# Performance work log

Hardware: AMD Instinct MI355X
Metric: run time of the kernel (lower is better)

The kernel has to match this reference:

```python
import jax, jax.numpy as jnp
import numpy as np

N = 20000
E = 320000
IN_DIM = 128
HID = 64
HEADS = 8
OUT_DIM = 128
NEG_SLOPE = 0.2  # PyG GATConv default leaky_relu slope


def _glorot(key, shape):
    fan_in = shape[0] if len(shape) > 1 else shape[-1]
    return jax.random.normal(key, shape, dtype=jnp.float32) / jnp.sqrt(jnp.float32(fan_in))


def setup_inputs() -> dict:
    key = jax.random.key(0)
    ks = jax.random.split(key, 16)
    x = jax.random.normal(ks[0], (N, IN_DIM), dtype=jnp.float32)
    edge_index = jax.random.randint(ks[1], (2, E), 0, N, dtype=jnp.int32)
    HC = HEADS * HID
    return {
        "x": x,
        "edge_index": edge_index,
        # layer 1: in -> heads*hid (concat)
        "W1": _glorot(ks[2], (IN_DIM, HC)),
        "a_src1": _glorot(ks[3], (HEADS, HID)),
        "a_dst1": _glorot(ks[4], (HEADS, HID)),
        "b1": jnp.zeros((HC,), jnp.float32),
        # layer 2: heads*hid -> heads*hid (concat)
        "W2": _glorot(ks[5], (HC, HC)),
        "a_src2": _glorot(ks[6], (HEADS, HID)),
        "a_dst2": _glorot(ks[7], (HEADS, HID)),
        "b2": jnp.zeros((HC,), jnp.float32),
        # layer 3: heads*hid -> out, heads=1, concat=False
        "W3": _glorot(ks[8], (HC, OUT_DIM)),
        "a_src3": _glorot(ks[9], (1, OUT_DIM)),
        "a_dst3": _glorot(ks[10], (1, OUT_DIM)),
        "b3": jnp.zeros((OUT_DIM,), jnp.float32),
    }


def _gat_layer(x, src, dst, W, a_src, a_dst, b, heads, concat):
    # x: [N, F_in] -> h: [N, H, C]
    n = x.shape[0]
    h = (x @ W).reshape(n, heads, -1)
    # per-node attention half-logits: [N, H]
    al_src = jnp.sum(h * a_src[None], axis=-1)
    al_dst = jnp.sum(h * a_dst[None], axis=-1)
    # per-edge logits with leaky relu: [E, H]
    e = jax.nn.leaky_relu(al_src[src] + al_dst[dst], NEG_SLOPE)
    # segment softmax over incoming edges of each dst node
    emax = jax.ops.segment_max(e, dst, num_segments=n)
    ex = jnp.exp(e - emax[dst])
    den = jax.ops.segment_sum(ex, dst, num_segments=n)
    alpha = ex / (den[dst] + 1e-16)
    # weighted scatter-aggregate of source features: [E, H, C] -> [N, H, C]
    out = jax.ops.segment_sum(h[src] * alpha[:, :, None], dst, num_segments=n)
    out = out.reshape(n, -1) if concat else out.mean(axis=1)
    return out + b


def reference(x, edge_index, W1, a_src1, a_dst1, b1, W2, a_src2, a_dst2, b2,
              W3, a_src3, a_dst3, b3):
    # PyG GATConv adds self-loops by default
    loops = jnp.arange(N, dtype=edge_index.dtype)
    src = jnp.concatenate([edge_index[0], loops])
    dst = jnp.concatenate([edge_index[1], loops])
    # eval mode: dropout is identity
    h = _gat_layer(x, src, dst, W1, a_src1, a_dst1, b1, HEADS, True)
    h = jax.nn.elu(h)
    h = _gat_layer(h, src, dst, W2, a_src2, a_dst2, b2, HEADS, True)
    h = jax.nn.elu(h)
    out = _gat_layer(h, src, dst, W3, a_src3, a_dst3, b3, 1, False)
    return out
```

## Files before the change

kernel.cpp:

```cpp
#include <hip/hip_runtime.h>
#include <math.h>

#define NN 20000
#define EE 320000
#define ETOT 340000
#define NHEADS 8
#define HID 64
#define HCV 512
#define IND 128
#define OUTD 128
#define NEG_SLOPE 0.2f

typedef __attribute__((ext_vector_type(8))) _Float16 half8;
typedef __attribute__((ext_vector_type(4))) float floatx4;

__device__ __forceinline__ void cvt_one(const float* W, _Float16* T, int idx, int K, int N) {
    int k = idx / N, n = idx - k * N;
    T[(size_t)n * K + k] = (_Float16)W[idx];
}

#define S1 (IND * HCV)
#define S2 (HCV * HCV)
#define S3 (HCV * OUTD)
#define STOT (S1 + S2 + S3)
#define XTOT (NN * IND)
__global__ void prep_kernel(const float* __restrict__ W1, const float* __restrict__ W2,
                            const float* __restrict__ W3, const float* __restrict__ x,
                            const float* __restrict__ as1, const float* __restrict__ ad1,
                            _Float16* __restrict__ T1, _Float16* __restrict__ T2,
                            _Float16* __restrict__ T3, _Float16* __restrict__ xh,
                            float* __restrict__ w1p, int* __restrict__ cnt) {
    int idx = blockIdx.x * blockDim.x + threadIdx.x;
    if (idx < S1) cvt_one(W1, T1, idx, IND, HCV);
    else if (idx < S1 + S2) cvt_one(W2, T2, idx - S1, HCV, HCV);
    else if (idx < STOT) cvt_one(W3, T3, idx - S1 - S2, HCV, OUTD);
    else if (idx < STOT + NN) cnt[idx - STOT] = 0;
    else if (idx < STOT + NN + XTOT) {
        int j = idx - STOT - NN;
        xh[j] = (_Float16)x[j];
    } else if (idx < STOT + NN + XTOT + IND * 16) {
        int j = idx - STOT - NN - XTOT;
        int c = j >> 4, o = j & 15;
        int hh = o & 7;
        const float* av = (o < 8) ? as1 : ad1;
        float s = 0.f;
        #pragma unroll 8
        for (int jj = 0; jj < HID; jj++)
            s = fmaf(W1[c * HCV + hh * HID + jj], av[hh * HID + jj], s);
        w1p[c * 16 + o] = s;
    }
}


__global__ void count_kernel(const int* __restrict__ ei, int* __restrict__ cnt) {
    int i = blockIdx.x * blockDim.x + threadIdx.x;
    if (i >= ETOT) return;
    int v = (i < EE) ? ei[EE + i] : (i - EE);
    atomicAdd(&cnt[v], 1);
}

#define SCH 20
__global__ __launch_bounds__(1024) void scan_kernel(const int* __restrict__ cnt,
                                                    int* __restrict__ row_ptr,
                                                    int* __restrict__ cursor) {
    __shared__ int wtot[16];
    __shared__ int woff[16];
    int t = threadIdx.x;
    int lane = t & 63;
    int wid = t >> 6;
    int base = t * SCH;
    int vals[SCH];
    int s = 0;
    #pragma unroll
    for (int i = 0; i < SCH; i++) {
        int idx = base + i;
        int v = (idx < NN) ? cnt[idx] : 0;
        vals[i] = v;
        s += v;
    }
    int incl = s;
    #pragma unroll
    for (int off = 1; off < 64; off <<= 1) {
        int u = __shfl_up(incl, off);
        if (lane >= off) incl += u;
    }
    int excl = incl - s;
    if (lane == 63) wtot[wid] = incl;
    __syncthreads();
    if (t == 0) {
        int run = 0;
        #pragma unroll
        for (int j = 0; j < 16; j++) { woff[j] = run; run += wtot[j]; }
        row_ptr[NN] = run;
    }
    __syncthreads();
    int run = woff[wid] + excl;
    #pragma unroll
    for (int i = 0; i < SCH; i++) {
        int idx = base + i;
        if (idx < NN) { row_ptr[idx] = run; cursor[idx] = run; run += vals[i]; }
    }
}

__global__ void fill_kernel(const int* __restrict__ ei, int* __restrict__ cursor,
                            int* __restrict__ csr_src) {
    int i = blockIdx.x * blockDim.x + threadIdx.x;
    if (i >= ETOT) return;
    int u, v;
    if (i < EE) { u = ei[i]; v = ei[EE + i]; }
    else        { u = i - EE; v = i - EE; }
    int pos = atomicAdd(&cursor[v], 1);
    csr_src[pos] = u;
}

__global__ void al1_thin(const float* __restrict__ x, const float* __restrict__ w1p,
                         float* __restrict__ als, float* __restrict__ ald) {
    int gid = blockIdx.x * blockDim.x + threadIdx.x;
    int node = gid >> 4, o = gid & 15;
    if (node >= NN) return;
    const float* xr = x + (size_t)node * IND;
    float s = 0.f;
    #pragma unroll 4
    for (int c = 0; c < IND; c++)
        s = fmaf(xr[c], w1p[c * 16 + o], s);
    if (o < 8) als[node * 8 + o] = s;
    else       ald[node * 8 + (o - 8)] = s;
}

__global__ __launch_bounds__(256) void gather1_kernel(const _Float16* __restrict__ xh,
                                                      const int* __restrict__ row_ptr,
                                                      const int* __restrict__ csr_src,
                                                      const float* __restrict__ als,
                                                      const float* __restrict__ ald,
                                                      _Float16* __restrict__ xagg) {
    int lane = threadIdx.x & 63;
    int v = blockIdx.x * 4 + (threadIdx.x >> 6);
    if (v >= NN) return;
    int hd = lane >> 3;
    int cg = lane & 7;
    float adst = ald[v * NHEADS + hd];
    int s0 = row_ptr[v], s1 = row_ptr[v + 1];
    float acc[16] = {};
    float l = 0.f;
    int i = s0;
    for (; i + 2 <= s1; i += 2) {
        int u0 = csr_src[i], u1 = csr_src[i + 1];
        float t0 = als[u0 * NHEADS + hd] + adst;
        float t1 = als[u1 * NHEADS + hd] + adst;
        t0 = (t0 > 0.f) ? t0 : NEG_SLOPE * t0;
        t1 = (t1 > 0.f) ? t1 : NEG_SLOPE * t1;
        float p0 = __expf(fminf(t0, 80.f));
        float p1 = __expf(fminf(t1, 80.f));
        half8 a0 = *(const half8*)&xh[(size_t)u0 * IND + cg * 16];
        half8 b0 = *(const half8*)&xh[(size_t)u0 * IND + cg * 16 + 8];
        half8 a1 = *(const half8*)&xh[(size_t)u1 * IND + cg * 16];
        half8 b1 = *(const half8*)&xh[(size_t)u1 * IND + cg * 16 + 8];
        l += p0 + p1;
        #pragma unroll
        for (int j = 0; j < 8; j++) {
            acc[j]     = fmaf(p0, (float)a0[j], acc[j]);
            acc[j + 8] = fmaf(p0, (float)b0[j], acc[j + 8]);
            acc[j]     = fmaf(p1, (float)a1[j], acc[j]);
            acc[j + 8] = fmaf(p1, (float)b1[j], acc[j + 8]);
        }
    }
    if (i < s1) {
        int u0 = csr_src[i];
        float t0 = als[u0 * NHEADS + hd] + adst;
        t0 = (t0 > 0.f) ? t0 : NEG_SLOPE * t0;
        float p0 = __expf(fminf(t0, 80.f));
        half8 a0 = *(const half8*)&xh[(size_t)u0 * IND + cg * 16];
        half8 b0 = *(const half8*)&xh[(size_t)u0 * IND + cg * 16 + 8];
        l += p0;
        #pragma unroll
        for (int j = 0; j < 8; j++) {
            acc[j]     = fmaf(p0, (float)a0[j], acc[j]);
            acc[j + 8] = fmaf(p0, (float)b0[j], acc[j + 8]);
        }
    }
    float inv = 1.f / (l + 1e-16f);
    half8 o0, o1;
    #pragma unroll
    for (int j = 0; j < 8; j++) {
        o0[j] = (_Float16)(acc[j] * inv);
        o1[j] = (_Float16)(acc[j + 8] * inv);
    }
    size_t base = (size_t)v * (NHEADS * IND) + hd * IND + cg * 16;
    *(half8*)&xagg[base] = o0;
    *(half8*)&xagg[base + 8] = o1;
}

#define LDK 40
__global__ __launch_bounds__(256) void gemm1_bd(const _Float16* __restrict__ xagg,
                                                const _Float16* __restrict__ Bt,
                                                const float* __restrict__ bias,
                                                _Float16* __restrict__ gact,
                                                int M) {
    __shared__ _Float16 sA[64 * LDK];
    __shared__ _Float16 sB[64 * LDK];
    int tid = threadIdx.x;
    int lane = tid & 63;
    int wv = tid >> 6;
    int m0 = blockIdx.x * 64;
    int h = blockIdx.y;
    int quad = lane >> 4;
    int l15 = lane & 15;
    int arow = tid >> 2;
    int ac4 = tid & 3;

    floatx4 acc[4] = {};

    for (int k0 = 0; k0 < IND; k0 += 32) {
        {
            int gm = m0 + arow;
            int4 va;
            if (gm < M) va = *(const int4*)&xagg[(size_t)gm * (NHEADS * IND) + h * IND + k0 + ac4 * 8];
            else        va = make_int4(0, 0, 0, 0);
            *(int4*)&sA[arow * LDK + ac4 * 8] = va;
            int gn = h * 64 + arow;
            int4 vb = *(const int4*)&Bt[(size_t)gn * IND + k0 + ac4 * 8];
            *(int4*)&sB[arow * LDK + ac4 * 8] = vb;
        }
        __syncthreads();
        half8 a[4], b;
        #pragma unroll
        for (int i = 0; i < 4; i++)
            a[i] = *(const half8*)&sA[(i * 16 + l15) * LDK + quad * 8];
        b = *(const half8*)&sB[(wv * 16 + l15) * LDK + quad * 8];
        #pragma unroll
        for (int i = 0; i < 4; i++)
            acc[i] = __builtin_amdgcn_mfma_f32_16x16x32_f16(a[i], b, acc[i], 0, 0, 0);
        __syncthreads();
    }
    #pragma unroll
    for (int i = 0; i < 4; i++) {
        #pragma unroll
        for (int r = 0; r < 4; r++) {
            int gm = m0 + i * 16 + quad * 4 + r;
            if (gm < M) {
                int col = h * 64 + wv * 16 + l15;
                float o = acc[i][r] + bias[col];
                o = (o > 0.f) ? o : (__expf(o) - 1.f);
                gact[(size_t)gm * HCV + col] = (_Float16)o;
            }
        }
    }
}

__global__ __launch_bounds__(256) void gemm_l2(const _Float16* __restrict__ A,
                                               const _Float16* __restrict__ Bt,
                                               _Float16* __restrict__ C16,
                                               const float* __restrict__ a_src,
                                               const float* __restrict__ a_dst,
                                               float* __restrict__ als,
                                               float* __restrict__ ald,
                                               int M, int K) {
    __shared__ _Float16 sA[64 * LDK];
    __shared__ _Float16 sB[128 * LDK];
    __shared__ float psum_s[4][64];
    __shared__ float psum_d[4][64];
    int tid = threadIdx.x;
    int lane = tid & 63;
    int wv = tid >> 6;
    int m0 = blockIdx.x * 64, n0 = blockIdx.y * 128;
    int quad = lane >> 4;
    int l15 = lane & 15;
    int arow = tid >> 2;
    int ac4 = tid & 3;

    floatx4 acc[4][2] = {};

    for (int k0 = 0; k0 < K; k0 += 32) {
        {
            int gm = m0 + arow;
            int4 va;
            if (gm < M) va = *(const int4*)&A[(size_t)gm * K + k0 + ac4 * 8];
            else        va = make_int4(0, 0, 0, 0);
            *(int4*)&sA[arow * LDK + ac4 * 8] = va;
            #pragma unroll
            for (int r = 0; r < 2; r++) {
                int gn = n0 + arow + r * 64;
                int4 vb = *(const int4*)&Bt[(size_t)gn * K + k0 + ac4 * 8];
                *(int4*)&sB[(arow + r * 64) * LDK + ac4 * 8] = vb;
            }
        }
        __syncthreads();
        half8 a[4], b[2];
        #pragma unroll
        for (int i = 0; i < 4; i++)
            a[i] = *(const half8*)&sA[(i * 16 + l15) * LDK + quad * 8];
        #pragma unroll
        for (int j = 0; j < 2; j++)
            b[j] = *(const half8*)&sB[(wv * 32 + j * 16 + l15) * LDK + quad * 8];
        #pragma unroll
        for (int i = 0; i < 4; i++)
            #pragma unroll
            for (int j = 0; j < 2; j++)
                acc[i][j] = __builtin_amdgcn_mfma_f32_16x16x32_f16(a[i], b[j], acc[i][j], 0, 0, 0);
        __syncthreads();
    }
    #pragma unroll
    for (int i = 0; i < 4; i++) {
        #pragma unroll
        for (int r = 0; r < 4; r++) {
            int gm = m0 + i * 16 + quad * 4 + r;
            if (gm < M) {
                #pragma unroll
                for (int j = 0; j < 2; j++)
                    C16[(size_t)gm * HCV + n0 + wv * 32 + j * 16 + l15] = (_Float16)acc[i][j][r];
            }
        }
    }
    int h0 = n0 >> 6;
    float as_v[2], ad_v[2];
    #pragma unroll
    for (int j = 0; j < 2; j++) {
        int dim = (wv * 32 + j * 16 + l15) & 63;
        int hh = h0 + (wv >> 1);
        as_v[j] = a_src[hh * HID + dim];
        ad_v[j] = a_dst[hh * HID + dim];
    }
    #pragma unroll
    for (int i = 0; i < 4; i++) {
        #pragma unroll
        for (int r = 0; r < 4; r++) {
            float ps = acc[i][0][r] * as_v[0] + acc[i][1][r] * as_v[1];
            float pd = acc[i][0][r] * ad_v[0] + acc[i][1][r] * ad_v[1];
            #pragma unroll
            for (int off = 1; off <= 8; off <<= 1) {
                ps += __shfl_xor(ps, off);
                pd += __shfl_xor(pd, off);
            }
            if (l15 == 0) {
                int row = i * 16 + quad * 4 + r;
                psum_s[wv][row] = ps;
                psum_d[wv][row] = pd;
            }
        }
    }
    __syncthreads();
    if (tid < 64) {
        int gm = m0 + tid;
        if (gm < M) {
            als[gm * NHEADS + h0]     = psum_s[0][tid] + psum_s[1][tid];
            als[gm * NHEADS + h0 + 1] = psum_s[2][tid] + psum_s[3][tid];
            ald[gm * NHEADS + h0]     = psum_d[0][tid] + psum_d[1][tid];
            ald[gm * NHEADS + h0 + 1] = psum_d[2][tid] + psum_d[3][tid];
        }
    }
}

__global__ __launch_bounds__(256) void gemm3(const _Float16* __restrict__ A,
                                             const _Float16* __restrict__ Bt,
                                             _Float16* __restrict__ C16,
                                             const float* __restrict__ a_src,
                                             const float* __restrict__ a_dst,
                                             float* __restrict__ als,
                                             float* __restrict__ ald,
                                             int M, int K) {
    __shared__ _Float16 sA[64 * LDK];
    __shared__ _Float16 sB[128 * LDK];
    __shared__ float psum_s[4][64];
    __shared__ float psum_d[4][64];
    int tid = threadIdx.x;
    int lane = tid & 63;
    int wv = tid >> 6;
    int m0 = blockIdx.x * 64;
    int quad = lane >> 4;
    int l15 = lane & 15;
    int arow = tid >> 2;
    int ac4 = tid & 3;

    floatx4 acc[4][2] = {};

    for (int k0 = 0; k0 < K; k0 += 32) {
        {
            int gm = m0 + arow;
            int4 va;
            if (gm < M) va = *(const int4*)&A[(size_t)gm * K + k0 + ac4 * 8];
            else        va = make_int4(0, 0, 0, 0);
            *(int4*)&sA[arow * LDK + ac4 * 8] = va;
            #pragma unroll
            for (int r = 0; r < 2; r++) {
                int gn = arow + r * 64;
                int4 vb = *(const int4*)&Bt[(size_t)gn * K + k0 + ac4 * 8];
                *(int4*)&sB[(arow + r * 64) * LDK + ac4 * 8] = vb;
            }
        }
        __syncthreads();
        half8 a[4], b[2];
        #pragma unroll
        for (int i = 0; i < 4; i++)
            a[i] = *(const half8*)&sA[(i * 16 + l15) * LDK + quad * 8];
        #pragma unroll
        for (int j = 0; j < 2; j++)
            b[j] = *(const half8*)&sB[(wv * 32 + j * 16 + l15) * LDK + quad * 8];
        #pragma unroll
        for (int i = 0; i < 4; i++)
            #pragma unroll
            for (int j = 0; j < 2; j++)
                acc[i][j] = __builtin_amdgcn_mfma_f32_16x16x32_f16(a[i], b[j], acc[i][j], 0, 0, 0);
        __syncthreads();
    }
    #pragma unroll
    for (int i = 0; i < 4; i++) {
        #pragma unroll
        for (int r = 0; r < 4; r++) {
            int gm = m0 + i * 16 + quad * 4 + r;
            if (gm < M) {
                #pragma unroll
                for (int j = 0; j < 2; j++)
                    C16[(size_t)gm * OUTD + wv * 32 + j * 16 + l15] = (_Float16)acc[i][j][r];
            }
        }
    }
    float as_v[2], ad_v[2];
    #pragma unroll
    for (int j = 0; j < 2; j++) {
        as_v[j] = a_src[wv * 32 + j * 16 + l15];
        ad_v[j] = a_dst[wv * 32 + j * 16 + l15];
    }
    #pragma unroll
    for (int i = 0; i < 4; i++) {
        #pragma unroll
        for (int r = 0; r < 4; r++) {
            float ps = acc[i][0][r] * as_v[0] + acc[i][1][r] * as_v[1];
            float pd = acc[i][0][r] * ad_v[0] + acc[i][1][r] * ad_v[1];
            #pragma unroll
            for (int off = 1; off <= 8; off <<= 1) {
                ps += __shfl_xor(ps, off);
                pd += __shfl_xor(pd, off);
            }
            if (l15 == 0) {
                int row = i * 16 + quad * 4 + r;
                psum_s[wv][row] = ps;
                psum_d[wv][row] = pd;
            }
        }
    }
    __syncthreads();
    if (tid < 64) {
        int gm = m0 + tid;
        if (gm < M) {
            als[gm] = psum_s[0][tid] + psum_s[1][tid] + psum_s[2][tid] + psum_s[3][tid];
            ald[gm] = psum_d[0][tid] + psum_d[1][tid] + psum_d[2][tid] + psum_d[3][tid];
        }
    }
}

__global__ __launch_bounds__(256) void gather2_kernel(const _Float16* __restrict__ h,
                                                      const int* __restrict__ row_ptr,
                                                      const int* __restrict__ csr_src,
                                                      const float* __restrict__ als,
                                                      const float* __restrict__ ald,
                                                      const float* __restrict__ bias,
                                                      _Float16* __restrict__ gout) {
    int lane = threadIdx.x & 63;
    int v = blockIdx.x * 4 + (threadIdx.x >> 6);
    if (v >= NN) return;
    int hd = lane >> 3;
    float adst = ald[v * NHEADS + hd];
    int s0 = row_ptr[v], s1 = row_ptr[v + 1];
    float acc[8] = {};
    float l = 0.f;
    int i = s0;
    for (; i + 4 <= s1; i += 4) {
        int u0 = csr_src[i], u1 = csr_src[i + 1], u2 = csr_src[i + 2], u3 = csr_src[i + 3];
        float t0 = als[u0 * NHEADS + hd] + adst;
        float t1 = als[u1 * NHEADS + hd] + adst;
        float t2 = als[u2 * NHEADS + hd] + adst;
        float t3 = als[u3 * NHEADS + hd] + adst;
        t0 = (t0 > 0.f) ? t0 : NEG_SLOPE * t0;
        t1 = (t1 > 0.f) ? t1 : NEG_SLOPE * t1;
        t2 = (t2 > 0.f) ? t2 : NEG_SLOPE * t2;
        t3 = (t3 > 0.f) ? t3 : NEG_SLOPE * t3;
        float p0 = __expf(fminf(t0, 80.f));
        float p1 = __expf(fminf(t1, 80.f));
        float p2 = __expf(fminf(t2, 80.f));
        float p3 = __expf(fminf(t3, 80.f));
        half8 x0 = *(const half8*)&h[(size_t)u0 * HCV + lane * 8];
        half8 x1 = *(const half8*)&h[(size_t)u1 * HCV + lane * 8];
        half8 x2 = *(const half8*)&h[(size_t)u2 * HCV + lane * 8];
        half8 x3 = *(const half8*)&h[(size_t)u3 * HCV + lane * 8];
        l += (p0 + p1) + (p2 + p3);
        #pragma unroll
        for (int j = 0; j < 8; j++) {
            acc[j] = fmaf(p0, (float)x0[j], acc[j]);
            acc[j] = fmaf(p1, (float)x1[j], acc[j]);
            acc[j] = fmaf(p2, (float)x2[j], acc[j]);
            acc[j] = fmaf(p3, (float)x3[j], acc[j]);
        }
    }
    for (; i < s1; i++) {
        int u0 = csr_src[i];
        float t0 = als[u0 * NHEADS + hd] + adst;
        t0 = (t0 > 0.f) ? t0 : NEG_SLOPE * t0;
        float p0 = __expf(fminf(t0, 80.f));
        half8 x0 = *(const half8*)&h[(size_t)u0 * HCV + lane * 8];
        l += p0;
        #pragma unroll
        for (int j = 0; j < 8; j++)
            acc[j] = fmaf(p0, (float)x0[j], acc[j]);
    }
    float inv = 1.f / (l + 1e-16f);
    half8 hv;
    #pragma unroll
    for (int j = 0; j < 8; j++) {
        float o = fmaf(acc[j], inv, bias[lane * 8 + j]);
        o = (o > 0.f) ? o : (__expf(o) - 1.f);
        hv[j] = (_Float16)o;
    }
    *(half8*)&gout[(size_t)v * HCV + lane * 8] = hv;
}

__global__ __launch_bounds__(256) void gather3_kernel(const _Float16* __restrict__ h,
                                                      const int* __restrict__ row_ptr,
                                                      const int* __restrict__ csr_src,
                                                      const float* __restrict__ als,
                                                      const float* __restrict__ ald,
                                                      const float* __restrict__ bias,
                                                      float* __restrict__ out) {
    int lane = threadIdx.x & 63;
    int v = blockIdx.x * 4 + (threadIdx.x >> 6);
    if (v >= NN) return;
    int e_sub = lane >> 4;
    int cg = lane & 15;
    float adst = ald[v];
    int s0 = row_ptr[v], s1 = row_ptr[v + 1];
    float m = -INFINITY;
    for (int i = s0 + e_sub; i < s1; i += 4) {
        int u = csr_src[i];
        float t = als[u] + adst;
        t = (t > 0.f) ? t : NEG_SLOPE * t;
        m = fmaxf(m, t);
    }
    m = fmaxf(m, __shfl_xor(m, 16));
    m = fmaxf(m, __shfl_xor(m, 32));
    float acc[8] = {};
    float l = 0.f;
    for (int i = s0 + e_sub; i < s1; i += 4) {
        int u = csr_src[i];
        float t = als[u] + adst;
        t = (t > 0.f) ? t : NEG_SLOPE * t;
        float p = __expf(t - m);
        half8 x = *(const half8*)&h[(size_t)u * OUTD + cg * 8];
        l += p;
        #pragma unroll
        for (int j = 0; j < 8; j++)
            acc[j] = fmaf(p, (float)x[j], acc[j]);
    }
    l += __shfl_xor(l, 16);
    l += __shfl_xor(l, 32);
    #pragma unroll
    for (int j = 0; j < 8; j++) {
        acc[j] += __shfl_xor(acc[j], 16);
        acc[j] += __shfl_xor(acc[j], 32);
    }
    if (e_sub == 0) {
        float inv = 1.f / (l + 1e-16f);
        float4 o0, o1;
        o0.x = fmaf(acc[0], inv, bias[cg * 8 + 0]);
        o0.y = fmaf(acc[1], inv, bias[cg * 8 + 1]);
        o0.z = fmaf(acc[2], inv, bias[cg * 8 + 2]);
        o0.w = fmaf(acc[3], inv, bias[cg * 8 + 3]);
        o1.x = fmaf(acc[4], inv, bias[cg * 8 + 4]);
        o1.y = fmaf(acc[5], inv, bias[cg * 8 + 5]);
        o1.z = fmaf(acc[6], inv, bias[cg * 8 + 6]);
        o1.w = fmaf(acc[7], inv, bias[cg * 8 + 7]);
        *(float4*)&out[(size_t)v * OUTD + cg * 8] = o0;
        *(float4*)&out[(size_t)v * OUTD + cg * 8 + 4] = o1;
    }
}


extern "C" void kernel_launch(void* const* d_in, const int* in_sizes, int n_in,
                              void* d_out, int out_size, void* d_ws, size_t ws_size,
                              hipStream_t stream) {
    const float* x     = (const float*)d_in[0];
    const int*   ei    = (const int*)d_in[1];
    const float* W1    = (const float*)d_in[2];
    const float* as1   = (const float*)d_in[3];
    const float* ad1   = (const float*)d_in[4];
    const float* b1    = (const float*)d_in[5];
    const float* W2    = (const float*)d_in[6];
    const float* as2   = (const float*)d_in[7];
    const float* ad2   = (const float*)d_in[8];
    const float* b2    = (const float*)d_in[9];
    const float* W3    = (const float*)d_in[10];
    const float* as3   = (const float*)d_in[11];
    const float* ad3   = (const float*)d_in[12];
    const float* b3    = (const float*)d_in[13];
    float* out = (float*)d_out;

    size_t off = 0;
    auto carve = [&](size_t bytes) {
        void* p = (char*)d_ws + off;
        off += (bytes + 255) & ~(size_t)255;
        return p;
    };
    int* row_ptr   = (int*)carve((NN + 1) * sizeof(int));
    int* cursor    = (int*)carve(NN * sizeof(int));
    int* csr_src   = (int*)carve(ETOT * sizeof(int));
    _Float16* xh   = (_Float16*)carve((size_t)NN * IND * sizeof(_Float16));
    _Float16* xagg = (_Float16*)carve((size_t)NN * NHEADS * IND * sizeof(_Float16));
    _Float16* gact = (_Float16*)carve((size_t)NN * HCV * sizeof(_Float16));
    _Float16* hf16 = (_Float16*)carve((size_t)NN * HCV * sizeof(_Float16));
    _Float16* h3   = (_Float16*)carve((size_t)NN * OUTD * sizeof(_Float16));
    float* als     = (float*)carve((size_t)NN * NHEADS * sizeof(float));
    float* ald     = (float*)carve((size_t)NN * NHEADS * sizeof(float));
    float* w1p     = (float*)carve((size_t)IND * 16 * sizeof(float));
    _Float16* W1T  = (_Float16*)carve((size_t)S1 * sizeof(_Float16));
    _Float16* W2T  = (_Float16*)carve((size_t)S2 * sizeof(_Float16));
    _Float16* W3T  = (_Float16*)carve((size_t)S3 * sizeof(_Float16));
    _Float16* gact2 = xagg;
    (void)ws_size; (void)n_in; (void)in_sizes; (void)out_size;

    dim3 blk(256);

    int prep_n = STOT + NN + XTOT + IND * 16;
    prep_kernel<<<(prep_n + 255) / 256, blk, 0, stream>>>(W1, W2, W3, x, as1, ad1,
        W1T, W2T, W3T, xh, w1p, cursor);

    count_kernel<<<(ETOT + 255) / 256, blk, 0, stream>>>(ei, cursor);
    scan_kernel<<<1, 1024, 0, stream>>>(cursor, row_ptr, cursor);
    fill_kernel<<<(ETOT + 255) / 256, blk, 0, stream>>>(ei, cursor, csr_src);

    int mt64 = (NN + 63) / 64;
    int nwaves_n = (NN + 3) / 4;

    al1_thin<<<(NN * 16 + 255) / 256, blk, 0, stream>>>(x, w1p, als, ald);
    gather1_kernel<<<nwaves_n, blk, 0, stream>>>(xh, row_ptr, csr_src, als, ald, xagg);
    gemm1_bd<<<dim3(mt64, NHEADS), blk, 0, stream>>>(xagg, W1T, b1, gact, NN);

    gemm_l2<<<dim3(mt64, HCV / 128), blk, 0, stream>>>(gact, W2T, hf16, as2, ad2, als, ald, NN, HCV);
    gather2_kernel<<<nwaves_n, blk, 0, stream>>>(hf16, row_ptr, csr_src, als, ald, b2, gact2);

    gemm3<<<dim3(mt64, 1), blk, 0, stream>>>(gact2, W3T, h3, as3, ad3, als, ald, NN, HCV);
    gather3_kernel<<<nwaves_n, blk, 0, stream>>>(h3, row_ptr, csr_src, als, ald, b3, out);
}
```

Measured before the change: 346.3 us.

## Split each node's edge list across four waves in gather1 and gather2

```diff
diff --git a/kernel.cpp b/kernel.cpp
--- a/kernel.cpp
+++ b/kernel.cpp
@@ -12,6 +12,8 @@
 #define NEG_SLOPE 0.2f
 
 typedef __attribute__((ext_vector_type(8))) _Float16 half8;
+typedef __attribute__((ext_vector_type(4))) _Float16 half4;
+typedef __attribute__((ext_vector_type(2))) _Float16 half2v;
 typedef __attribute__((ext_vector_type(4))) float floatx4;
 
 __device__ __forceinline__ void cvt_one(const float* W, _Float16* T, int idx, int K, int N) {
@@ -133,61 +135,64 @@
                                                       const float* __restrict__ als,
                                                       const float* __restrict__ ald,
                                                       _Float16* __restrict__ xagg) {
-    int lane = threadIdx.x & 63;
-    int v = blockIdx.x * 4 + (threadIdx.x >> 6);
-    if (v >= NN) return;
+    __shared__ float sacc[4][NHEADS * IND];
+    __shared__ float sl[4][NHEADS];
+    int tid = threadIdx.x;
+    int lane = tid & 63;
+    int w = tid >> 6;
+    int v = blockIdx.x;
     int hd = lane >> 3;
     int cg = lane & 7;
     float adst = ald[v * NHEADS + hd];
     int s0 = row_ptr[v], s1 = row_ptr[v + 1];
     float acc[16] = {};
     float l = 0.f;
-    int i = s0;
-    for (; i + 2 <= s1; i += 2) {
-        int u0 = csr_src[i], u1 = csr_src[i + 1];
-        float t0 = als[u0 * NHEADS + hd] + adst;
-        float t1 = als[u1 * NHEADS + hd] + adst;
-        t0 = (t0 > 0.f) ? t0 : NEG_SLOPE * t0;
-        t1 = (t1 > 0.f) ? t1 : NEG_SLOPE * t1;
-        float p0 = __expf(fminf(t0, 80.f));
-        float p1 = __expf(fminf(t1, 80.f));
-        half8 a0 = *(const half8*)&xh[(size_t)u0 * IND + cg * 16];
-        half8 b0 = *(const half8*)&xh[(size_t)u0 * IND + cg * 16 + 8];
-        half8 a1 = *(const half8*)&xh[(size_t)u1 * IND + cg * 16];
-        half8 b1 = *(const half8*)&xh[(size_t)u1 * IND + cg * 16 + 8];
-        l += p0 + p1;
-        #pragma unroll
-        for (int j = 0; j < 8; j++) {
-            acc[j]     = fmaf(p0, (float)a0[j], acc[j]);
-            acc[j + 8] = fmaf(p0, (float)b0[j], acc[j + 8]);
-            acc[j]     = fmaf(p1, (float)a1[j], acc[j]);
-            acc[j + 8] = fmaf(p1, (float)b1[j], acc[j + 8]);
-        }
-    }
-    if (i < s1) {
-        int u0 = csr_src[i];
-        float t0 = als[u0 * NHEADS + hd] + adst;
-        t0 = (t0 > 0.f) ? t0 : NEG_SLOPE * t0;
-        float p0 = __expf(fminf(t0, 80.f));
-        half8 a0 = *(const half8*)&xh[(size_t)u0 * IND + cg * 16];
-        half8 b0 = *(const half8*)&xh[(size_t)u0 * IND + cg * 16 + 8];
-        l += p0;
-        #pragma unroll
-        for (int j = 0; j < 8; j++) {
-            acc[j]     = fmaf(p0, (float)a0[j], acc[j]);
-            acc[j + 8] = fmaf(p0, (float)b0[j], acc[j + 8]);
-        }
-    }
-    float inv = 1.f / (l + 1e-16f);
-    half8 o0, o1;
-    #pragma unroll
-    for (int j = 0; j < 8; j++) {
-        o0[j] = (_Float16)(acc[j] * inv);
-        o1[j] = (_Float16)(acc[j + 8] * inv);
-    }
-    size_t base = (size_t)v * (NHEADS * IND) + hd * IND + cg * 16;
-    *(half8*)&xagg[base] = o0;
-    *(half8*)&xagg[base + 8] = o1;
+    for (int i = s0 + w * 2; i < s1; i += 8) {
+        {
+            int u0 = csr_src[i];
+            float t0 = als[u0 * NHEADS + hd] + adst;
+            t0 = (t0 > 0.f) ? t0 : NEG_SLOPE * t0;
+            float p0 = __expf(fminf(t0, 80.f));
+            half8 a0 = *(const half8*)&xh[(size_t)u0 * IND + cg * 16];
+            half8 b0 = *(const half8*)&xh[(size_t)u0 * IND + cg * 16 + 8];
+            l += p0;
+            #pragma unroll
+            for (int j = 0; j < 8; j++) {
+                acc[j]     = fmaf(p0, (float)a0[j], acc[j]);
+                acc[j + 8] = fmaf(p0, (float)b0[j], acc[j + 8]);
+            }
+        }
+        if (i + 1 < s1) {
+            int u1 = csr_src[i + 1];
+            float t1 = als[u1 * NHEADS + hd] + adst;
+            t1 = (t1 > 0.f) ? t1 : NEG_SLOPE * t1;
+            float p1 = __expf(fminf(t1, 80.f));
+            half8 a1 = *(const half8*)&xh[(size_t)u1 * IND + cg * 16];
+            half8 b1 = *(const half8*)&xh[(size_t)u1 * IND + cg * 16 + 8];
+            l += p1;
+            #pragma unroll
+            for (int j = 0; j < 8; j++) {
+                acc[j]     = fmaf(p1, (float)a1[j], acc[j]);
+                acc[j + 8] = fmaf(p1, (float)b1[j], acc[j + 8]);
+            }
+        }
+    }
+    #pragma unroll
+    for (int j = 0; j < 16; j++)
+        sacc[w][hd * IND + cg * 16 + j] = acc[j];
+    if (cg == 0) sl[w][hd] = l;
+    __syncthreads();
+    int ch = tid * 4;
+    int hh = ch >> 7;
+    float lt = sl[0][hh] + sl[1][hh] + sl[2][hh] + sl[3][hh];
+    float inv = 1.f / (lt + 1e-16f);
+    half4 o;
+    #pragma unroll
+    for (int j = 0; j < 4; j++) {
+        float a = sacc[0][ch + j] + sacc[1][ch + j] + sacc[2][ch + j] + sacc[3][ch + j];
+        o[j] = (_Float16)(a * inv);
+    }
+    *(half4*)&xagg[(size_t)v * (NHEADS * IND) + ch] = o;
 }
 
 #define LDK 40
@@ -455,62 +460,59 @@
                                                       const float* __restrict__ ald,
                                                       const float* __restrict__ bias,
                                                       _Float16* __restrict__ gout) {
-    int lane = threadIdx.x & 63;
-    int v = blockIdx.x * 4 + (threadIdx.x >> 6);
-    if (v >= NN) return;
+    __shared__ float sacc[4][HCV];
+    __shared__ float sl[4][NHEADS];
+    int tid = threadIdx.x;
+    int lane = tid & 63;
+    int w = tid >> 6;
+    int v = blockIdx.x;
     int hd = lane >> 3;
     float adst = ald[v * NHEADS + hd];
     int s0 = row_ptr[v], s1 = row_ptr[v + 1];
     float acc[8] = {};
     float l = 0.f;
-    int i = s0;
-    for (; i + 4 <= s1; i += 4) {
-        int u0 = csr_src[i], u1 = csr_src[i + 1], u2 = csr_src[i + 2], u3 = csr_src[i + 3];
-        float t0 = als[u0 * NHEADS + hd] + adst;
-        float t1 = als[u1 * NHEADS + hd] + adst;
-        float t2 = als[u2 * NHEADS + hd] + adst;
-        float t3 = als[u3 * NHEADS + hd] + adst;
-        t0 = (t0 > 0.f) ? t0 : NEG_SLOPE * t0;
-        t1 = (t1 > 0.f) ? t1 : NEG_SLOPE * t1;
-        t2 = (t2 > 0.f) ? t2 : NEG_SLOPE * t2;
-        t3 = (t3 > 0.f) ? t3 : NEG_SLOPE * t3;
-        float p0 = __expf(fminf(t0, 80.f));
-        float p1 = __expf(fminf(t1, 80.f));
-        float p2 = __expf(fminf(t2, 80.f));
-        float p3 = __expf(fminf(t3, 80.f));
-        half8 x0 = *(const half8*)&h[(size_t)u0 * HCV + lane * 8];
-        half8 x1 = *(const half8*)&h[(size_t)u1 * HCV + lane * 8];
-        half8 x2 = *(const half8*)&h[(size_t)u2 * HCV + lane * 8];
-        half8 x3 = *(const half8*)&h[(size_t)u3 * HCV + lane * 8];
-        l += (p0 + p1) + (p2 + p3);
-        #pragma unroll
-        for (int j = 0; j < 8; j++) {
-            acc[j] = fmaf(p0, (float)x0[j], acc[j]);
-            acc[j] = fmaf(p1, (float)x1[j], acc[j]);
-            acc[j] = fmaf(p2, (float)x2[j], acc[j]);
-            acc[j] = fmaf(p3, (float)x3[j], acc[j]);
-        }
-    }
-    for (; i < s1; i++) {
-        int u0 = csr_src[i];
-        float t0 = als[u0 * NHEADS + hd] + adst;
-        t0 = (t0 > 0.f) ? t0 : NEG_SLOPE * t0;
-        float p0 = __expf(fminf(t0, 80.f));
-        half8 x0 = *(const half8*)&h[(size_t)u0 * HCV + lane * 8];
-        l += p0;
-        #pragma unroll
-        for (int j = 0; j < 8; j++)
-            acc[j] = fmaf(p0, (float)x0[j], acc[j]);
-    }
-    float inv = 1.f / (l + 1e-16f);
-    half8 hv;
-    #pragma unroll
-    for (int j = 0; j < 8; j++) {
-        float o = fmaf(acc[j], inv, bias[lane * 8 + j]);
-        o = (o > 0.f) ? o : (__expf(o) - 1.f);
-        hv[j] = (_Float16)o;
-    }
-    *(half8*)&gout[(size_t)v * HCV + lane * 8] = hv;
+    for (int i = s0 + w * 2; i < s1; i += 8) {
+        {
+            int u0 = csr_src[i];
+            float t0 = als[u0 * NHEADS + hd] + adst;
+            t0 = (t0 > 0.f) ? t0 : NEG_SLOPE * t0;
+            float p0 = __expf(fminf(t0, 80.f));
+            half8 x0 = *(const half8*)&h[(size_t)u0 * HCV + lane * 8];
+            l += p0;
+            #pragma unroll
+            for (int j = 0; j < 8; j++)
+                acc[j] = fmaf(p0, (float)x0[j], acc[j]);
+        }
+        if (i + 1 < s1) {
+            int u1 = csr_src[i + 1];
+            float t1 = als[u1 * NHEADS + hd] + adst;
+            t1 = (t1 > 0.f) ? t1 : NEG_SLOPE * t1;
+            float p1 = __expf(fminf(t1, 80.f));
+            half8 x1 = *(const half8*)&h[(size_t)u1 * HCV + lane * 8];
+            l += p1;
+            #pragma unroll
+            for (int j = 0; j < 8; j++)
+                acc[j] = fmaf(p1, (float)x1[j], acc[j]);
+        }
+    }
+    #pragma unroll
+    for (int j = 0; j < 8; j++)
+        sacc[w][lane * 8 + j] = acc[j];
+    if ((lane & 7) == 0) sl[w][hd] = l;
+    __syncthreads();
+    int ch = tid * 2;
+    int hh = ch >> 6;
+    float lt = sl[0][hh] + sl[1][hh] + sl[2][hh] + sl[3][hh];
+    float inv = 1.f / (lt + 1e-16f);
+    half2v o;
+    #pragma unroll
+    for (int j = 0; j < 2; j++) {
+        float a = sacc[0][ch + j] + sacc[1][ch + j] + sacc[2][ch + j] + sacc[3][ch + j];
+        float ov = fmaf(a, inv, bias[ch + j]);
+        ov = (ov > 0.f) ? ov : (__expf(ov) - 1.f);
+        o[j] = (_Float16)ov;
+    }
+    *(half2v*)&gout[(size_t)v * HCV + ch] = o;
 }
 
 __global__ __launch_bounds__(256) void gather3_kernel(const _Float16* __restrict__ h,
@@ -629,11 +631,11 @@
     int nwaves_n = (NN + 3) / 4;
 
     al1_thin<<<(NN * 16 + 255) / 256, blk, 0, stream>>>(x, w1p, als, ald);
-    gather1_kernel<<<nwaves_n, blk, 0, stream>>>(xh, row_ptr, csr_src, als, ald, xagg);
+    gather1_kernel<<<NN, blk, 0, stream>>>(xh, row_ptr, csr_src, als, ald, xagg);
     gemm1_bd<<<dim3(mt64, NHEADS), blk, 0, stream>>>(xagg, W1T, b1, gact, NN);
 
     gemm_l2<<<dim3(mt64, HCV / 128), blk, 0, stream>>>(gact, W2T, hf16, as2, ad2, als, ald, NN, HCV);
-    gather2_kernel<<<nwaves_n, blk, 0, stream>>>(hf16, row_ptr, csr_src, als, ald, b2, gact2);
+    gather2_kernel<<<NN, blk, 0, stream>>>(hf16, row_ptr, csr_src, als, ald, b2, gact2);
 
     gemm3<<<dim3(mt64, 1), blk, 0, stream>>>(gact2, W3T, h3, as3, ad3, als, ald, NN, HCV);
     gather3_kernel<<<nwaves_n, blk, 0, stream>>>(h3, row_ptr, csr_src, als, ald, b3, out);
```

Result: slower. 358.5 us (+3.5%).
